# Kernel tuning notes

Measured on AMD Instinct MI355X. Metric: run time of the kernel, lower is better.

## Reference

```python
import jax, jax.numpy as jnp
import numpy as np

EPS = 1e-5
NEG_SLOPE = 0.2

def _bn(x, g, b, m, v):
    # eval-mode BatchNorm over channel axis 1
    sh = (1, -1) + (1,) * (x.ndim - 2)
    inv = g.reshape(sh) * jax.lax.rsqrt(v.reshape(sh) + EPS)
    return (x - m.reshape(sh)) * inv + b.reshape(sh)

def _lrelu(x):
    return jnp.where(x >= 0, x, NEG_SLOPE * x)

def _edge_feature(x, idx):
    # x: [B,C,N], idx: [B,N,k] -> edge diffs [B,C,N,k]
    xT = jnp.transpose(x, (0, 2, 1))                      # [B,N,C]
    B = x.shape[0]
    neigh = xT[jnp.arange(B)[:, None, None], idx]         # [B,N,k,C]
    e = neigh - xT[:, :, None, :]                         # [B,N,k,C]
    return jnp.transpose(e, (0, 3, 1, 2))                 # [B,C,N,k]

def _edgeconv(x, idx, w, g, b, m, v):
    e = _edge_feature(x, idx)                             # [B,Cin,N,k]
    y = jnp.einsum('bcnk,oc->bonk', e, w)                 # 1x1 conv2d, no bias
    y = _lrelu(_bn(y, g, b, m, v))
    return jnp.max(y, axis=-1)                            # max over k -> [B,Cout,N]

def _pointconv(x, w, g, b, m, v):
    y = jnp.einsum('bcn,oc->bon', x, w)                   # 1x1 conv1d, no bias
    return _lrelu(_bn(y, g, b, m, v))

def setup_inputs() -> dict:
    key = jax.random.key(0)
    B, N, K = 8, 4096, 20
    ks = jax.random.split(key, 40)
    it = iter(range(40))
    d = {}
    d['x'] = jax.random.normal(ks[next(it)], (B, 3, N), dtype=jnp.float32)
    d['idx'] = jax.random.randint(ks[next(it)], (B, N, K), 0, N, dtype=jnp.int32)
    dims = [(64, 3), (64, 64), (128, 64), (256, 128), (256, 512), (128, 256), (1, 128)]
    for i, (o, c) in enumerate(dims, 1):
        d[f'w{i}'] = jax.random.normal(ks[next(it)], (o, c), dtype=jnp.float32) * (1.0 / np.sqrt(c))
    for i, c in enumerate([64, 64, 128, 256, 256, 128], 1):
        d[f'g{i}'] = jax.random.uniform(ks[next(it)], (c,), dtype=jnp.float32, minval=0.5, maxval=1.5)
        d[f'b{i}'] = jax.random.normal(ks[next(it)], (c,), dtype=jnp.float32) * 0.1
        d[f'm{i}'] = jax.random.normal(ks[next(it)], (c,), dtype=jnp.float32) * 0.1
        d[f'v{i}'] = jax.random.uniform(ks[next(it)], (c,), dtype=jnp.float32, minval=0.5, maxval=1.5)
    return d

def reference(x, idx, w1, w2, w3, w4, w5, w6, w7,
              g1, b1, m1, v1, g2, b2, m2, v2, g3, b3, m3, v3,
              g4, b4, m4, v4, g5, b5, m5, v5, g6, b6, m6, v6):
    x1 = _edgeconv(x,  idx, w1, g1, b1, m1, v1)   # [B,64,N]
    x2 = _edgeconv(x1, idx, w2, g2, b2, m2, v2)   # [B,64,N]
    x3 = _edgeconv(x2, idx, w3, g3, b3, m3, v3)   # [B,128,N]
    x4 = _edgeconv(x3, idx, w4, g4, b4, m4, v4)   # [B,256,N]
    h = jnp.concatenate((x1, x2, x3, x4), axis=1) # [B,512,N]
    h = _pointconv(h, w5, g5, b5, m5, v5)         # [B,256,N]
    h = _pointconv(h, w6, g6, b6, m6, v6)         # [B,128,N]
    h = _lrelu(jnp.einsum('bcn,oc->bon', h, w7))  # [B,1,N]
    return jnp.transpose(h, (0, 2, 1))            # [B,N,1]
```

## Files before the change

### kernel.cpp

```cpp
#include <hip/hip_runtime.h>
#include <hip/hip_bf16.h>
#include <cstdint>
#include <cstddef>

#define EPS 1e-5f
#define NEG 0.2f

static constexpr int B_ = 8, N_ = 4096, K_ = 20, M_ = B_ * N_;

typedef __attribute__((ext_vector_type(8))) _Float16 f16x8;
typedef __attribute__((ext_vector_type(4))) float f32x4;

#define VMCNT(n) asm volatile("s_waitcnt vmcnt(" #n ")" ::: "memory")

__device__ __forceinline__ void gload_lds16(const _Float16* g, _Float16* l) {
  __builtin_amdgcn_global_load_lds(
      (const __attribute__((address_space(1))) uint32_t*)g,
      (__attribute__((address_space(3))) uint32_t*)l, 16, 0, 0);
}

__global__ __launch_bounds__(256) void prep_c3(
    const float* __restrict__ x, const float* __restrict__ w1,
    const float* __restrict__ w2, const float* __restrict__ w3,
    const float* __restrict__ w4, const float* __restrict__ w5,
    const float* __restrict__ w6,
    const float* __restrict__ g1, const float* __restrict__ b1, const float* __restrict__ m1, const float* __restrict__ v1,
    const float* __restrict__ g2, const float* __restrict__ b2, const float* __restrict__ m2, const float* __restrict__ v2,
    const float* __restrict__ g3, const float* __restrict__ b3, const float* __restrict__ m3, const float* __restrict__ v3,
    const float* __restrict__ g4, const float* __restrict__ b4, const float* __restrict__ m4, const float* __restrict__ v4,
    const float* __restrict__ g5, const float* __restrict__ b5, const float* __restrict__ m5, const float* __restrict__ v5,
    const float* __restrict__ g6, const float* __restrict__ b6, const float* __restrict__ m6, const float* __restrict__ v6,
    float* __restrict__ P, _Float16* __restrict__ Wh, _Float16* __restrict__ z) {
  const int bid = blockIdx.x, tid = threadIdx.x;
  if (bid < 512) {
    const int o  = tid & 63;
    const int pi = tid >> 6;
    const float ww0 = w1[o * 3 + 0], ww1 = w1[o * 3 + 1], ww2 = w1[o * 3 + 2];
    const float iv = g1[o] * rsqrtf(v1[o] + EPS);
    const int pbase = bid * 64;
    const int b = pbase >> 12;
    const int nbase = pbase & (N_ - 1);
    const float* xb = x + (size_t)b * 3 * N_;
    for (int pj = pi; pj < 64; pj += 4) {
      const int n = nbase + pj;
      const float x0 = xb[n], x1v = xb[N_ + n], x2v = xb[2 * N_ + n];
      z[(size_t)(pbase + pj) * 64 + o] = (_Float16)((x0 * ww0 + x1v * ww1 + x2v * ww2) * iv);
    }
    return;
  }
  if (bid == 1328) {
    const float* G[6]  = {g1, g2, g3, g4, g5, g6};
    const float* Bb[6] = {b1, b2, b3, b4, b5, b6};
    const float* Mm[6] = {m1, m2, m3, m4, m5, m6};
    const float* Vv[6] = {v1, v2, v3, v4, v5, v6};
    const int Cs[6] = {64, 64, 128, 256, 256, 128};
    const int OI[6] = {0, 128, 256, 512, 1024, 1536};
    const int OB[6] = {64, 192, 384, 768, 1280, 1664};
    for (int l = 0; l < 6; ++l) {
      for (int c = tid; c < Cs[l]; c += 256) {
        float iv = G[l][c] * rsqrtf(Vv[l][c] + EPS);
        P[OI[l] + c] = iv;
        P[OB[l] + c] = Bb[l][c] - Mm[l][c] * iv;
      }
    }
    return;
  }
  const int fb = bid - 512;
  const float* w; const float* g; const float* v; _Float16* dst; int lc, base;
  if (fb < 16)       { w = w2; g = g2; v = v2; dst = Wh + 0;      lc = 6; base = 0;   }
  else if (fb < 48)  { w = w3; g = g3; v = v3; dst = Wh + 4096;   lc = 6; base = 16;  }
  else if (fb < 176) { w = w4; g = g4; v = v4; dst = Wh + 12288;  lc = 7; base = 48;  }
  else if (fb < 688) { w = w5; g = g5; v = v5; dst = Wh + 45056;  lc = 9; base = 176; }
  else               { w = w6; g = g6; v = v6; dst = Wh + 176128; lc = 8; base = 688; }
  const int e = (fb - base) * 256 + tid;
  const int o = e >> lc;
  dst[e] = (_Float16)(w[e] * (g[o] * rsqrtf(v[o] + EPS)));
}

template <int BO>
__global__ __launch_bounds__(256) void edge_gemm64(
    const _Float16* __restrict__ z, const int* __restrict__ idx,
    const float* __restrict__ betap,
    const _Float16* __restrict__ W,
    _Float16* __restrict__ hout,
    _Float16* __restrict__ zout, int ldzout) {
  constexpr int GW = BO / 8;
  constexpr int OJ = BO / 32;
  __shared__ _Float16 Asmem[128 * 64];
  __shared__ _Float16 Wsmem[BO * 64];

  const int tid = threadIdx.x, lane = tid & 63, wid = tid >> 6;
  const int batch = blockIdx.x & 7, chunk = blockIdx.x >> 3;
  const int bm0 = (batch << 12) + chunk * 128;
  const int lr = lane & 15, lk = lane >> 4;

  const _Float16* Wbase = W + (size_t)lr * 64 + lk * 8;
#pragma unroll
  for (int g = wid; g < GW; g += 4) {
    const int o = g >> 1, s = g & 1;
    gload_lds16(Wbase + (size_t)16 * o * 64 + s * 32, Wsmem + g * 512);
  }

  const int lid = tid & 7, cb = lid * 8;
  float bt[8];
#pragma unroll
  for (int q = 0; q < 8; ++q) bt[q] = betap[cb + q];
  const _Float16* zb = z + ((size_t)(batch << 12)) * 64;
#pragma unroll
  for (int pass = 0; pass < 4; ++pass) {
    const int pi = pass * 32 + (tid >> 3);
    const int p = bm0 + pi;
    const int* ip = idx + (size_t)p * K_;
    const int ir0 = ip[lid];
    const int ir1 = ip[8 + lid];
    const int ir2 = ip[16 + (lid & 3)];
    f16x8 mx = *reinterpret_cast<const f16x8*>(zb + (size_t)__shfl(ir0, 0, 8) * 64 + cb);
#pragma unroll
    for (int k = 1; k < K_; ++k) {
      const int g = (k < 8) ? __shfl(ir0, k, 8)
                  : (k < 16) ? __shfl(ir1, k - 8, 8)
                             : __shfl(ir2, k - 16, 8);
      const f16x8 v = *reinterpret_cast<const f16x8*>(zb + (size_t)g * 64 + cb);
#pragma unroll
      for (int q = 0; q < 8; ++q) mx[q] = v[q] > mx[q] ? v[q] : mx[q];
    }
    const f16x8 vc = *reinterpret_cast<const f16x8*>(z + (size_t)p * 64 + cb);
    f16x8 vo;
#pragma unroll
    for (int q = 0; q < 8; ++q) {
      const float e = (float)mx[q] - (float)vc[q] + bt[q];
      vo[q] = (_Float16)fmaxf(e, NEG * e);
    }
    *reinterpret_cast<f16x8*>(hout + (size_t)p * 512 + cb) = vo;
    const int i = pi >> 4, rr = pi & 15, s = cb >> 5, kk = (cb >> 3) & 3;
    *reinterpret_cast<f16x8*>(Asmem + (i * 2 + s) * 512 + ((kk << 4) | rr) * 8) = vo;
  }
  __syncthreads();

  const int wr = wid >> 1, wc = wid & 1;
  f32x4 acc[4][OJ];
#pragma unroll
  for (int i = 0; i < 4; ++i)
#pragma unroll
    for (int j = 0; j < OJ; ++j) acc[i][j] = (f32x4){0.f, 0.f, 0.f, 0.f};
#pragma unroll
  for (int s = 0; s < 2; ++s) {
    f16x8 av[4], wv[OJ];
#pragma unroll
    for (int i = 0; i < 4; ++i)
      av[i] = *reinterpret_cast<const f16x8*>(Asmem + ((wr * 4 + i) * 2 + s) * 512 + lane * 8);
#pragma unroll
    for (int j = 0; j < OJ; ++j)
      wv[j] = *reinterpret_cast<const f16x8*>(Wsmem + ((wc * OJ + j) * 2 + s) * 512 + lane * 8);
#pragma unroll
    for (int i = 0; i < 4; ++i)
#pragma unroll
      for (int j = 0; j < OJ; ++j)
        acc[i][j] = __builtin_amdgcn_mfma_f32_16x16x32_f16(av[i], wv[j], acc[i][j], 0, 0, 0);
  }

#pragma unroll
  for (int j = 0; j < OJ; ++j) {
    const int o = wc * (BO / 2) + 16 * j + lr;
#pragma unroll
    for (int i = 0; i < 4; ++i) {
      const int r0 = bm0 + wr * 64 + 16 * i + lk * 4;
#pragma unroll
      for (int q = 0; q < 4; ++q)
        zout[(size_t)(r0 + q) * ldzout + o] = (_Float16)acc[i][j][q];
    }
  }
}

__global__ __launch_bounds__(512, 1) void edge_gemm_l4(
    const _Float16* __restrict__ z3,
    const int* __restrict__ idx,
    const float* __restrict__ btE,
    const _Float16* __restrict__ W4,
    _Float16* __restrict__ h512,
    _Float16* __restrict__ z4out) {
  constexpr int SB = 24 * 512;
  __shared__ _Float16 lds[4 * SB];

  const int tid = threadIdx.x, lane = tid & 63, wid = tid >> 6;
  const int wr = wid >> 2, wc = wid & 3;
  const int bid = blockIdx.x, batch = bid & 7;
  const int bm0 = (batch << 12) + (bid >> 3) * 128;
  const int lr = lane & 15, lk = lane >> 4;

  const _Float16* Wb = W4 + (size_t)lr * 128 + lk * 8;
#pragma unroll
  for (int q = 0; q < 8; ++q) {
    const int gg = wid * 8 + q;
    const int ob = gg >> 2, kk = gg & 3;
    gload_lds16(Wb + (size_t)16 * ob * 128 + kk * 32, &lds[kk * SB + (8 + ob) * 512]);
  }

  const int lid = tid & 15, cb = lid * 8;
  float bt[8];
#pragma unroll
  for (int q = 0; q < 8; ++q) bt[q] = btE[cb + q];
  const _Float16* zb = z3 + ((size_t)(batch << 12)) * 128;
  f16x8 x3r[4];
#pragma unroll
  for (int pass = 0; pass < 4; ++pass) {
    const int pi = pass * 32 + (tid >> 4);
    const int p = bm0 + pi;
    const int* ip = idx + (size_t)p * K_;
    const int ir0 = ip[lid];
    const int ir1 = (lid < 4) ? ip[16 + lid] : 0;
    f16x8 mx = *reinterpret_cast<const f16x8*>(zb + (size_t)__shfl(ir0, 0, 16) * 128 + cb);
#pragma unroll
    for (int k = 1; k < K_; ++k) {
      const int g = (k < 16) ? __shfl(ir0, k, 16) : __shfl(ir1, k - 16, 16);
      const f16x8 v = *reinterpret_cast<const f16x8*>(zb + (size_t)g * 128 + cb);
#pragma unroll
      for (int q = 0; q < 8; ++q) mx[q] = v[q] > mx[q] ? v[q] : mx[q];
    }
    const f16x8 vc = *reinterpret_cast<const f16x8*>(z3 + (size_t)p * 128 + cb);
    f16x8 vo;
#pragma unroll
    for (int q = 0; q < 8; ++q) {
      const float e = (float)mx[q] - (float)vc[q] + bt[q];
      vo[q] = (_Float16)fmaxf(e, NEG * e);
    }
    x3r[pass] = vo;
    *reinterpret_cast<f16x8*>(h512 + (size_t)p * 512 + 128 + cb) = vo;
  }
  {
    const int kk = (cb >> 3) & 3;
    const int ts = cb >> 5;
    const int rr = (tid >> 4) & 15;
#pragma unroll
    for (int pp = 0; pp < 4; ++pp) {
      const int grp = pp * 2 + (tid >> 8);
      *reinterpret_cast<f16x8*>(&lds[ts * SB + grp * 512 + ((kk << 4) | rr) * 8]) = x3r[pp];
    }
  }
  __syncthreads();

  f32x4 acc[4][4];
#pragma unroll
  for (int i = 0; i < 4; ++i)
#pragma unroll
    for (int j = 0; j < 4; ++j) acc[i][j] = (f32x4){0.f, 0.f, 0.f, 0.f};
#pragma unroll
  for (int t = 0; t < 4; ++t) {
    f16x8 av[4], wv[4];
#pragma unroll
    for (int i = 0; i < 4; ++i)
      av[i] = *reinterpret_cast<const f16x8*>(&lds[t * SB + (wr * 4 + i) * 512 + lane * 8]);
#pragma unroll
    for (int j = 0; j < 4; ++j)
      wv[j] = *reinterpret_cast<const f16x8*>(&lds[t * SB + (8 + wc * 4 + j) * 512 + lane * 8]);
#pragma unroll
    for (int i = 0; i < 4; ++i)
#pragma unroll
      for (int j = 0; j < 4; ++j)
        acc[i][j] = __builtin_amdgcn_mfma_f32_16x16x32_f16(av[i], wv[j], acc[i][j], 0, 0, 0);
  }

#pragma unroll
  for (int j = 0; j < 4; ++j) {
    const int o = wc * 64 + 16 * j + lr;
#pragma unroll
    for (int i = 0; i < 4; ++i) {
      const int r0 = bm0 + wr * 64 + 16 * i + lk * 4;
#pragma unroll
      for (int q = 0; q < 4; ++q)
        z4out[(size_t)(r0 + q) * 256 + o] = (_Float16)acc[i][j][q];
    }
  }
}

template <int O>
__global__ __launch_bounds__(256) void edge_max8(
    const _Float16* __restrict__ z, const int* __restrict__ idx,
    const float* __restrict__ betap, _Float16* __restrict__ out, int ldout) {
  constexpr int TPP = O / 8;
  constexpr int PPB = 256 / TPP;
  constexpr int NW = (K_ + TPP - 1) / TPP;
  const int t = threadIdx.x;
  const int batch = blockIdx.x & 7;
  const int chunk = blockIdx.x >> 3;
  const int p = (batch << 12) + chunk * PPB + t / TPP;
  const int lid = t % TPP;
  const int cb = lid * 8;
  const int* ip = idx + (size_t)p * K_;
  int ir[NW];
#pragma unroll
  for (int wv = 0; wv < NW; ++wv) {
    const int l = wv * TPP + lid;
    ir[wv] = (l < K_) ? ip[l] : ip[0];
  }
  const _Float16* zb = z + ((size_t)(batch << 12)) * O;

  f16x8 mx = *reinterpret_cast<const f16x8*>(zb + (size_t)__shfl(ir[0], 0, TPP) * O + cb);
#pragma unroll
  for (int k = 1; k < K_; ++k) {
    const int g = __shfl(ir[k / TPP], k % TPP, TPP);
    const f16x8 v = *reinterpret_cast<const f16x8*>(zb + (size_t)g * O + cb);
#pragma unroll
    for (int q = 0; q < 8; ++q) mx[q] = v[q] > mx[q] ? v[q] : mx[q];
  }
  const f16x8 vc = *reinterpret_cast<const f16x8*>(z + (size_t)p * O + cb);
  f16x8 vo;
#pragma unroll
  for (int q = 0; q < 8; ++q) {
    const float e = (float)mx[q] - (float)vc[q] + betap[cb + q];
    vo[q] = (_Float16)fmaxf(e, NEG * e);
  }
  *reinterpret_cast<f16x8*>(out + (size_t)p * ldout + cb) = vo;
}

__global__ __launch_bounds__(512, 1) void gemm_l567(
    const _Float16* __restrict__ A,
    const _Float16* __restrict__ W5,
    const float* __restrict__ bt5,
    const _Float16* __restrict__ W6,
    const float* __restrict__ bt6,
    const float* __restrict__ w7,
    float* __restrict__ dout) {
  constexpr int SB = 24 * 512;
  constexpr int H5 = 4 * SB;
  __shared__ _Float16 lds[4 * SB + 32768];

  const int tid = threadIdx.x, lane = tid & 63, wid = tid >> 6;
  const int wr = wid >> 2, wc = wid & 3;
  const int bid = blockIdx.x;
  const int bm0 = ((bid & 7) << 12) + (bid >> 3) * 128;
  const int lr = lane & 15, lk = lane >> 4;

  const _Float16* Abase = A + (size_t)(bm0 + lr) * 512 + lk * 8;
  const _Float16* W5b = W5 + (size_t)lr * 512 + lk * 8;

  f32x4 acc[4][4];
#pragma unroll
  for (int i = 0; i < 4; ++i)
#pragma unroll
    for (int j = 0; j < 4; ++j) acc[i][j] = (f32x4){0.f, 0.f, 0.f, 0.f};

  auto stage = [&](int buf, int k0) {
    _Float16* dst = &lds[buf * SB];
#pragma unroll
    for (int q = 0; q < 3; ++q) {
      const int g = wid * 3 + q;
      const _Float16* src = (g < 8)
          ? Abase + (size_t)16 * g * 512 + k0
          : W5b + (size_t)16 * (g - 8) * 512 + k0;
      gload_lds16(src, dst + g * 512);
    }
  };

  stage(0, 0);
  stage(1, 32);
#pragma unroll
  for (int t = 0; t < 16; ++t) {
    if (t + 2 < 16) {
      stage((t + 2) & 3, (t + 2) * 32);
      VMCNT(6);
    } else if (t + 1 < 16) {
      VMCNT(3);
    } else {
      VMCNT(0);
    }
    __builtin_amdgcn_s_barrier();
    const _Float16* Ab = &lds[(t & 3) * SB];
    f16x8 av[4], wv[4];
#pragma unroll
    for (int i = 0; i < 4; ++i)
      av[i] = *reinterpret_cast<const f16x8*>(Ab + (wr * 4 + i) * 512 + lane * 8);
#pragma unroll
    for (int j = 0; j < 4; ++j)
      wv[j] = *reinterpret_cast<const f16x8*>(Ab + (8 + wc * 4 + j) * 512 + lane * 8);
#pragma unroll
    for (int i = 0; i < 4; ++i)
#pragma unroll
      for (int j = 0; j < 4; ++j)
        acc[i][j] = __builtin_amdgcn_mfma_f32_16x16x32_f16(av[i], wv[j], acc[i][j], 0, 0, 0);
  }

  {
    const _Float16* W6b = W6 + (size_t)lr * 256 + lk * 8;
#pragma unroll
    for (int q = 0; q < 8; ++q) {
      const int gg = wid * 8 + q;
      const int ob = gg >> 3, kk = gg & 7;
      gload_lds16(W6b + (size_t)16 * ob * 256 + kk * 32, &lds[gg * 512]);
    }
  }
#pragma unroll
  for (int j = 0; j < 4; ++j) {
    const int o = wc * 64 + 16 * j + lr;
    const float b5 = bt5[o];
    const int gcol = o >> 5;
    const int slotc = (o >> 3) & 3;
    const int elem = o & 7;
#pragma unroll
    for (int i = 0; i < 4; ++i) {
      const int rg = wr * 4 + i;
#pragma unroll
      for (int q = 0; q < 4; ++q) {
        const int rl = lk * 4 + q;
        float t = acc[i][j][q] + b5;
        t = fmaxf(t, NEG * t);
        lds[H5 + (rg * 8 + gcol) * 512 + (slotc * 16 + rl) * 8 + elem] = (_Float16)t;
      }
    }
  }
  __syncthreads();

  f32x4 acc2[4][2];
#pragma unroll
  for (int i = 0; i < 4; ++i)
#pragma unroll
    for (int j = 0; j < 2; ++j) acc2[i][j] = (f32x4){0.f, 0.f, 0.f, 0.f};
#pragma unroll
  for (int t = 0; t < 8; ++t) {
    f16x8 av[4], wv[2];
#pragma unroll
    for (int i = 0; i < 4; ++i)
      av[i] = *reinterpret_cast<const f16x8*>(&lds[H5 + ((wr * 4 + i) * 8 + t) * 512 + lane * 8]);
#pragma unroll
    for (int j = 0; j < 2; ++j)
      wv[j] = *reinterpret_cast<const f16x8*>(&lds[((wc * 2 + j) * 8 + t) * 512 + lane * 8]);
#pragma unroll
    for (int i = 0; i < 4; ++i)
#pragma unroll
      for (int j = 0; j < 2; ++j)
        acc2[i][j] = __builtin_amdgcn_mfma_f32_16x16x32_f16(av[i], wv[j], acc2[i][j], 0, 0, 0);
  }

  float* dotbuf = (float*)&lds[32768];
  float rowdot[4][4];
#pragma unroll
  for (int i = 0; i < 4; ++i)
#pragma unroll
    for (int q = 0; q < 4; ++q) rowdot[i][q] = 0.f;
#pragma unroll
  for (int j = 0; j < 2; ++j) {
    const int o = wc * 32 + 16 * j + lr;
    const float bt = bt6[o];
    const float wf = w7[o];
#pragma unroll
    for (int i = 0; i < 4; ++i)
#pragma unroll
      for (int q = 0; q < 4; ++q) {
        float t = acc2[i][j][q] + bt;
        t = fmaxf(t, NEG * t);
        rowdot[i][q] += t * wf;
      }
  }
#pragma unroll
  for (int i = 0; i < 4; ++i)
#pragma unroll
    for (int q = 0; q < 4; ++q) {
#pragma unroll
      for (int off = 1; off < 16; off <<= 1)
        rowdot[i][q] += __shfl_xor(rowdot[i][q], off, 16);
      if (lr == 0)
        dotbuf[(wr * 64 + 16 * i + lk * 4 + q) * 4 + wc] = rowdot[i][q];
    }
  __syncthreads();
  if (tid < 128) {
    const float s = dotbuf[tid * 4 + 0] + dotbuf[tid * 4 + 1] +
                    dotbuf[tid * 4 + 2] + dotbuf[tid * 4 + 3];
    dout[bm0 + tid] = fmaxf(s, NEG * s);
  }
}

extern "C" void kernel_launch(void* const* d_in, const int* in_sizes, int n_in,
                              void* d_out, int out_size, void* d_ws, size_t ws_size,
                              hipStream_t stream) {
  const float* x  = (const float*)d_in[0];
  const int* idx  = (const int*)d_in[1];
  const float* w[7];
  for (int i = 0; i < 7; ++i) w[i] = (const float*)d_in[2 + i];
  const float* bn[24];
  for (int i = 0; i < 24; ++i) bn[i] = (const float*)d_in[9 + i];

  float* P       = (float*)d_ws;
  _Float16* Wh   = (_Float16*)((char*)d_ws + (32 << 10));
  _Float16* z_a  = (_Float16*)((char*)d_ws + (1u << 20));
  _Float16* h512 = (_Float16*)((char*)d_ws + (17u << 20));
  _Float16* z_b  = (_Float16*)((char*)d_ws + (49u << 20));

  prep_c3<<<1329, 256, 0, stream>>>(
      x, w[0], w[1], w[2], w[3], w[4], w[5],
      bn[0], bn[1], bn[2], bn[3],   bn[4], bn[5], bn[6], bn[7],
      bn[8], bn[9], bn[10], bn[11], bn[12], bn[13], bn[14], bn[15],
      bn[16], bn[17], bn[18], bn[19], bn[20], bn[21], bn[22], bn[23],
      P, Wh, z_a);

  const float* bt1 = P + 64;
  const float* bt2 = P + 192;
  const float* bt3 = P + 384;
  const float* bt4 = P + 768;
  const float* bt5 = P + 1280;
  const float* bt6 = P + 1664;
  const _Float16* W2 = Wh + 0, *W3 = Wh + 4096, *W4 = Wh + 12288,
               *W5 = Wh + 45056, *W6 = Wh + 176128;

  edge_gemm64<64><<<M_ / 128, 256, 0, stream>>>(z_a, idx, bt1, W2, h512 + 0, z_b, 64);
  edge_gemm64<128><<<M_ / 128, 256, 0, stream>>>(z_b, idx, bt2, W3, h512 + 64, z_a, 128);
  edge_gemm_l4<<<M_ / 128, 512, 0, stream>>>(z_a, idx, bt3, W4, h512, z_b);
  edge_max8<256><<<M_ / 8, 256, 0, stream>>>(z_b, idx, bt4, h512 + 256, 512);
  gemm_l567<<<M_ / 128, 512, 0, stream>>>(
      h512, W5, bt5, W6, bt6, w[6], (float*)d_out);
}
```

Before: 90.61 us.

## Fuse layer-4 edge gather-max into the layer 5-7 GEMM kernel via LDS

Removes the separate edge_max8 kernel. The gather, max over neighbors and leaky-ReLU for layer 4 are now computed inside the final GEMM kernel, and the 256-channel result is written straight into LDS in MFMA operand layout. This avoids writing and re-reading the x4 slice of h512 through global memory, and saves one kernel launch. In exchange, the GEMM blocks do the irregular gather work up front before the MFMA loop, with only 256 blocks at occupancy 1, so gather latency may be less well hidden. The global-to-LDS staging and vmcnt waits are also retuned, since the second half of K now loads only weights.

```diff
diff --git a/kernel.cpp b/kernel.cpp
--- a/kernel.cpp
+++ b/kernel.cpp
@@ -273,48 +273,11 @@
   }
 }
 
-template <int O>
-__global__ __launch_bounds__(256) void edge_max8(
-    const _Float16* __restrict__ z, const int* __restrict__ idx,
-    const float* __restrict__ betap, _Float16* __restrict__ out, int ldout) {
-  constexpr int TPP = O / 8;
-  constexpr int PPB = 256 / TPP;
-  constexpr int NW = (K_ + TPP - 1) / TPP;
-  const int t = threadIdx.x;
-  const int batch = blockIdx.x & 7;
-  const int chunk = blockIdx.x >> 3;
-  const int p = (batch << 12) + chunk * PPB + t / TPP;
-  const int lid = t % TPP;
-  const int cb = lid * 8;
-  const int* ip = idx + (size_t)p * K_;
-  int ir[NW];
-#pragma unroll
-  for (int wv = 0; wv < NW; ++wv) {
-    const int l = wv * TPP + lid;
-    ir[wv] = (l < K_) ? ip[l] : ip[0];
-  }
-  const _Float16* zb = z + ((size_t)(batch << 12)) * O;
-
-  f16x8 mx = *reinterpret_cast<const f16x8*>(zb + (size_t)__shfl(ir[0], 0, TPP) * O + cb);
-#pragma unroll
-  for (int k = 1; k < K_; ++k) {
-    const int g = __shfl(ir[k / TPP], k % TPP, TPP);
-    const f16x8 v = *reinterpret_cast<const f16x8*>(zb + (size_t)g * O + cb);
-#pragma unroll
-    for (int q = 0; q < 8; ++q) mx[q] = v[q] > mx[q] ? v[q] : mx[q];
-  }
-  const f16x8 vc = *reinterpret_cast<const f16x8*>(z + (size_t)p * O + cb);
-  f16x8 vo;
-#pragma unroll
-  for (int q = 0; q < 8; ++q) {
-    const float e = (float)mx[q] - (float)vc[q] + betap[cb + q];
-    vo[q] = (_Float16)fmaxf(e, NEG * e);
-  }
-  *reinterpret_cast<f16x8*>(out + (size_t)p * ldout + cb) = vo;
-}
-
-__global__ __launch_bounds__(512, 1) void gemm_l567(
+__global__ __launch_bounds__(512, 1) void gemm_e4l567(
     const _Float16* __restrict__ A,
+    const _Float16* __restrict__ z4,
+    const int* __restrict__ idx,
+    const float* __restrict__ bt4,
     const _Float16* __restrict__ W5,
     const float* __restrict__ bt5,
     const _Float16* __restrict__ W6,
@@ -327,58 +290,106 @@
 
   const int tid = threadIdx.x, lane = tid & 63, wid = tid >> 6;
   const int wr = wid >> 2, wc = wid & 3;
-  const int bid = blockIdx.x;
-  const int bm0 = ((bid & 7) << 12) + (bid >> 3) * 128;
+  const int bid = blockIdx.x, batch = bid & 7;
+  const int bm0 = (batch << 12) + (bid >> 3) * 128;
   const int lr = lane & 15, lk = lane >> 4;
 
   const _Float16* Abase = A + (size_t)(bm0 + lr) * 512 + lk * 8;
   const _Float16* W5b = W5 + (size_t)lr * 512 + lk * 8;
 
+  auto stage = [&](int buf, int t) {
+    _Float16* dst = &lds[buf * SB];
+    if (t < 8) {
+#pragma unroll
+      for (int q = 0; q < 3; ++q) {
+        const int g = wid * 3 + q;
+        const _Float16* src = (g < 8)
+            ? Abase + (size_t)16 * g * 512 + t * 32
+            : W5b + (size_t)16 * (g - 8) * 512 + t * 32;
+        gload_lds16(src, dst + g * 512);
+      }
+    } else {
+#pragma unroll
+      for (int q = 0; q < 2; ++q) {
+        const int ob = wid * 2 + q;
+        gload_lds16(W5b + (size_t)16 * ob * 512 + t * 32, dst + (8 + ob) * 512);
+      }
+    }
+  };
+
+  stage(0, 0);
+  stage(1, 1);
+
+  {
+    const int lid = tid & 31, cb = lid * 8;
+    float bt[8];
+#pragma unroll
+    for (int q = 0; q < 8; ++q) bt[q] = bt4[cb + q];
+    const _Float16* zb = z4 + ((size_t)(batch << 12)) * 256;
+    const int ts8 = cb >> 5;
+    const int kk = (cb >> 3) & 3;
+#pragma unroll
+    for (int pass = 0; pass < 8; ++pass) {
+      const int pi = pass * 16 + (tid >> 5);
+      const int p = bm0 + pi;
+      const int* ip = idx + (size_t)p * K_;
+      const int ir = (lid < K_) ? ip[lid] : 0;
+      f16x8 mx = *reinterpret_cast<const f16x8*>(zb + (size_t)__shfl(ir, 0, 32) * 256 + cb);
+#pragma unroll
+      for (int k = 1; k < K_; ++k) {
+        const int g = __shfl(ir, k, 32);
+        const f16x8 v = *reinterpret_cast<const f16x8*>(zb + (size_t)g * 256 + cb);
+#pragma unroll
+        for (int q = 0; q < 8; ++q) mx[q] = v[q] > mx[q] ? v[q] : mx[q];
+      }
+      const f16x8 vc = *reinterpret_cast<const f16x8*>(z4 + (size_t)p * 256 + cb);
+      f16x8 vo;
+#pragma unroll
+      for (int q = 0; q < 8; ++q) {
+        const float e = (float)mx[q] - (float)vc[q] + bt[q];
+        vo[q] = (_Float16)fmaxf(e, NEG * e);
+      }
+      *reinterpret_cast<f16x8*>(
+          &lds[H5 + ts8 * 4096 + (pi >> 4) * 512 + ((kk << 4) | (pi & 15)) * 8]) = vo;
+    }
+  }
+  __syncthreads();
+
   f32x4 acc[4][4];
 #pragma unroll
   for (int i = 0; i < 4; ++i)
 #pragma unroll
     for (int j = 0; j < 4; ++j) acc[i][j] = (f32x4){0.f, 0.f, 0.f, 0.f};
 
-  auto stage = [&](int buf, int k0) {
-    _Float16* dst = &lds[buf * SB];
-#pragma unroll
-    for (int q = 0; q < 3; ++q) {
-      const int g = wid * 3 + q;
-      const _Float16* src = (g < 8)
-          ? Abase + (size_t)16 * g * 512 + k0
-          : W5b + (size_t)16 * (g - 8) * 512 + k0;
-      gload_lds16(src, dst + g * 512);
-    }
-  };
-
-  stage(0, 0);
-  stage(1, 32);
 #pragma unroll
   for (int t = 0; t < 16; ++t) {
     if (t + 2 < 16) {
-      stage((t + 2) & 3, (t + 2) * 32);
-      VMCNT(6);
+      stage((t + 2) & 3, t + 2);
+      if (t < 6)       VMCNT(6);
+      else if (t == 6) VMCNT(5);
+      else if (t < 14) VMCNT(4);
     } else if (t + 1 < 16) {
-      VMCNT(3);
+      VMCNT(2);
     } else {
       VMCNT(0);
     }
     __builtin_amdgcn_s_barrier();
-    const _Float16* Ab = &lds[(t & 3) * SB];
+    const _Float16* Ab = (t < 8) ? &lds[(t & 3) * SB] : &lds[H5 + (t - 8) * 4096];
+    const _Float16* Wb2 = &lds[(t & 3) * SB + 8 * 512];
     f16x8 av[4], wv[4];
 #pragma unroll
     for (int i = 0; i < 4; ++i)
       av[i] = *reinterpret_cast<const f16x8*>(Ab + (wr * 4 + i) * 512 + lane * 8);
 #pragma unroll
     for (int j = 0; j < 4; ++j)
-      wv[j] = *reinterpret_cast<const f16x8*>(Ab + (8 + wc * 4 + j) * 512 + lane * 8);
+      wv[j] = *reinterpret_cast<const f16x8*>(Wb2 + (wc * 4 + j) * 512 + lane * 8);
 #pragma unroll
     for (int i = 0; i < 4; ++i)
 #pragma unroll
       for (int j = 0; j < 4; ++j)
         acc[i][j] = __builtin_amdgcn_mfma_f32_16x16x32_f16(av[i], wv[j], acc[i][j], 0, 0, 0);
   }
+  __syncthreads();
 
   {
     const _Float16* W6b = W6 + (size_t)lr * 256 + lk * 8;
@@ -504,7 +515,6 @@
   edge_gemm64<64><<<M_ / 128, 256, 0, stream>>>(z_a, idx, bt1, W2, h512 + 0, z_b, 64);
   edge_gemm64<128><<<M_ / 128, 256, 0, stream>>>(z_b, idx, bt2, W3, h512 + 64, z_a, 128);
   edge_gemm_l4<<<M_ / 128, 512, 0, stream>>>(z_a, idx, bt3, W4, h512, z_b);
-  edge_max8<256><<<M_ / 8, 256, 0, stream>>>(z_b, idx, bt4, h512 + 256, 512);
-  gemm_l567<<<M_ / 128, 512, 0, stream>>>(
-      h512, W5, bt5, W6, bt6, w[6], (float*)d_out);
+  gemm_e4l567<<<M_ / 128, 512, 0, stream>>>(
+      h512, z_b, idx, bt4, W5, bt5, W6, bt6, w[6], (float*)d_out);
 }
```

New measurement: 93.77 us. 3.5% more time.
